# Kernel tuning notes

Hardware: AMD Instinct MI355X
Metric: run time of the kernel (lower is better)

## Reference

```python
import jax, jax.numpy as jnp
import numpy as np

INPUT, OUTPUT, HIDDEN, EMBED = 20000, 2048, 1024, 512
BATCH, NUM_GENES = 512, 20000

def _linear_init(key, fan_in, fan_out):
    kw, kb = jax.random.split(key)
    bound = 1.0 / np.sqrt(fan_in)
    W = jax.random.uniform(kw, (fan_out, fan_in), minval=-bound, maxval=bound, dtype=jnp.float32)
    b = jax.random.uniform(kb, (fan_out,), minval=-bound, maxval=bound, dtype=jnp.float32)
    return W, b

def setup_inputs() -> dict:
    key = jax.random.key(0)
    kx, ke, k1, k2, k3 = jax.random.split(key, 5)
    x = jax.random.normal(kx, (BATCH, INPUT), dtype=jnp.float32)
    embedding_x = jax.random.normal(ke, (NUM_GENES, EMBED), dtype=jnp.float32)
    W_ge, b_ge = _linear_init(k1, INPUT, HIDDEN)   # gene_expander Linear
    W_em, b_em = _linear_init(k2, EMBED, HIDDEN)   # embed_mlp Linear
    W_c, b_c = _linear_init(k3, 2 * HIDDEN, OUTPUT)  # combiner Linear
    return {"x": x, "embedding_x": embedding_x, "W_ge": W_ge, "b_ge": b_ge,
            "W_em": W_em, "b_em": b_em, "W_c": W_c, "b_c": b_c}

def reference(x, embedding_x, W_ge, b_ge, W_em, b_em, W_c, b_c):
    lrelu = lambda v: jax.nn.leaky_relu(v, negative_slope=0.01)
    # gene_expander: [B, input] -> [B, hidden]
    x_expanded = lrelu(x @ W_ge.T + b_ge)
    # embed_mlp (dropout = identity at eval): [G, embed] -> [G, hidden]
    gene_embeddings = lrelu(embedding_x @ W_em.T + b_em)
    # softmax over features, then batched GEMM replaces the per-sample loop
    num_genes = min(x.shape[1], gene_embeddings.shape[0])
    weights = jax.nn.softmax(x, axis=1)
    weighted_embeddings = weights[:, :num_genes] @ gene_embeddings[:num_genes]  # [B, hidden]
    combined = jnp.concatenate([x_expanded, weighted_embeddings], axis=1)  # [B, 2*hidden]
    return lrelu(combined @ W_c.T + b_c)  # [B, output]
```

## Files before the change

### kernel.cpp

```cpp
#include <hip/hip_runtime.h>
#include <hip/hip_bf16.h>
#include <stdint.h>

#define BATCH  512
#define INPUT  20000
#define KPAD   20032
#define NPADE  20224
#define HIDDEN 1024
#define EMBED  512
#define NOUT   2048

typedef __attribute__((ext_vector_type(8))) __bf16 bf16x8;
typedef __attribute__((ext_vector_type(8))) unsigned short u16x8;
typedef __attribute__((ext_vector_type(4))) unsigned short u16x4;
typedef __attribute__((ext_vector_type(4))) float f32x4;

static __device__ __forceinline__ unsigned short f2bf(float f) {
  uint32_t u = __builtin_bit_cast(uint32_t, f);
  u += 0x7fffu + ((u >> 16) & 1u);
  return (unsigned short)(u >> 16);
}

static __device__ __forceinline__ void g2l16(const unsigned short* g, unsigned short* l) {
  __builtin_amdgcn_global_load_lds(
      (const __attribute__((address_space(1))) void*)g,
      (__attribute__((address_space(3))) void*)l, 16, 0, 0);
}

#define MFMA(a, b, c) __builtin_amdgcn_mfma_f32_16x16x32_bf16((a), (b), (c), 0, 0, 0)

template<int EPI>
__global__ __launch_bounds__(512, 2) void gemm8p(
    const unsigned short* __restrict__ A0p, const unsigned short* __restrict__ B0p,
    const unsigned short* __restrict__ A1p, const unsigned short* __restrict__ B1p,
    int lda, int ldb,
    const float* __restrict__ bias,
    void* __restrict__ Cp, int ldc,
    int Nv, int Nw, int K, int kChunk)
{
  __shared__ __align__(16) unsigned short As[2][2][128 * 64];
  __shared__ __align__(16) unsigned short Bs[2][2][128 * 64];
  unsigned short* AsW = &As[0][0][0];
  unsigned short* BsW = &Bs[0][0][0];

  const int zall  = blockIdx.z;
  const int which = (EPI == 1) ? (zall >> 4) : 0;
  const int z     = (EPI == 1) ? (zall & 15) : 0;
  const unsigned short* Ap = which ? A1p : A0p;
  const unsigned short* Bp = which ? B1p : B0p;

  const int m0 = blockIdx.y * 256, n0 = blockIdx.x * 256;
  const int k0   = z * kChunk;
  const int kend = min(K, k0 + kChunk);
  const int nt   = (kend - k0) >> 6;

  const int tid = threadIdx.x;
  const int l = tid & 63, w = tid >> 6;
  const int srow = tid >> 3;
  const int scol = (((tid & 7) ^ (srow & 7)) << 3);

  const unsigned short* ag = Ap + (size_t)(m0 + srow) * lda + k0 + scol;
  const unsigned short* bg = Bp + (size_t)(n0 + srow) * ldb + k0 + scol;

  const int wr = w >> 2, wc = w & 3;
  const int lr = l & 15, lk = (l >> 4) * 8;
  const int xorv = (lr & 7) * 8;
  const int c0 = lk ^ xorv;
  const int c1 = (32 + lk) ^ xorv;

  auto stA = [&](int buf, int h, int dk) {
    const unsigned short* g = ag + (size_t)(h * 128) * lda + dk;
    unsigned short* d = AsW + (buf * 2 + h) * 8192 + (w * 8) * 64;
    g2l16(g, d);
    g2l16(g + (size_t)64 * lda, d + 64 * 64);
  };
  auto stB = [&](int buf, int h, int dk) {
    const unsigned short* g = bg + (size_t)(h * 128) * ldb + dk;
    unsigned short* d = BsW + (buf * 2 + h) * 8192 + (w * 8) * 64;
    g2l16(g, d);
    g2l16(g + (size_t)64 * ldb, d + 64 * 64);
  };
  auto rdA = [&](int buf, int mi, int ks) -> bf16x8 {
    return *reinterpret_cast<const bf16x8*>(
        AsW + (buf * 2 + wr) * 8192 + (mi * 16 + lr) * 64 + (ks ? c1 : c0));
  };
  auto rdB = [&](int buf, int ni, int ks) -> bf16x8 {
    return *reinterpret_cast<const bf16x8*>(
        BsW + (buf * 2 + (wc >> 1)) * 8192 + ((wc & 1) * 64 + ni * 16 + lr) * 64 + (ks ? c1 : c0));
  };

  f32x4 acc[8][4] = {};

  stA(0, 0, 0); stB(0, 0, 0); stA(0, 1, 0); stB(0, 1, 0);
  if (nt > 1) {
    stA(1, 0, 64); stB(1, 0, 64);
    asm volatile("s_waitcnt vmcnt(4)" ::: "memory");
  } else {
    asm volatile("s_waitcnt vmcnt(0)" ::: "memory");
  }
  __builtin_amdgcn_s_barrier();

  for (int t = 0; t < nt; ++t) {
    const int buf = t & 1, nb = buf ^ 1;
    const int dk1 = (t + 1) << 6, dk2 = (t + 2) << 6;
    bf16x8 a0[4][2], a1[4][2], b0[2][2], b1[2][2];

#pragma unroll
    for (int mi = 0; mi < 4; ++mi) { a0[mi][0] = rdA(buf, mi, 0); a0[mi][1] = rdA(buf, mi, 1); }
#pragma unroll
    for (int ni = 0; ni < 2; ++ni) { b0[ni][0] = rdB(buf, ni, 0); b0[ni][1] = rdB(buf, ni, 1); }
    if (t + 1 < nt) stA(nb, 1, dk1);
    __builtin_amdgcn_s_barrier();
    asm volatile("s_waitcnt lgkmcnt(0)" ::: "memory");
    __builtin_amdgcn_sched_barrier(0);
    __builtin_amdgcn_s_setprio(1);
#pragma unroll
    for (int mi = 0; mi < 4; ++mi)
#pragma unroll
      for (int ni = 0; ni < 2; ++ni) {
        acc[mi][ni] = MFMA(a0[mi][0], b0[ni][0], acc[mi][ni]);
        acc[mi][ni] = MFMA(a0[mi][1], b0[ni][1], acc[mi][ni]);
      }
    __builtin_amdgcn_s_setprio(0);
    __builtin_amdgcn_s_barrier();

#pragma unroll
    for (int mi = 0; mi < 4; ++mi) { a1[mi][0] = rdA(buf, mi + 4, 0); a1[mi][1] = rdA(buf, mi + 4, 1); }
    if (t + 1 < nt) stB(nb, 1, dk1);
    __builtin_amdgcn_s_barrier();
    asm volatile("s_waitcnt lgkmcnt(0)" ::: "memory");
    __builtin_amdgcn_sched_barrier(0);
    __builtin_amdgcn_s_setprio(1);
#pragma unroll
    for (int mi = 0; mi < 4; ++mi)
#pragma unroll
      for (int ni = 0; ni < 2; ++ni) {
        acc[mi + 4][ni] = MFMA(a1[mi][0], b0[ni][0], acc[mi + 4][ni]);
        acc[mi + 4][ni] = MFMA(a1[mi][1], b0[ni][1], acc[mi + 4][ni]);
      }
    __builtin_amdgcn_s_setprio(0);
    __builtin_amdgcn_s_barrier();

#pragma unroll
    for (int ni = 0; ni < 2; ++ni) { b1[ni][0] = rdB(buf, ni + 2, 0); b1[ni][1] = rdB(buf, ni + 2, 1); }
    if (t + 2 < nt) stA(buf, 0, dk2);
    __builtin_amdgcn_s_barrier();
    asm volatile("s_waitcnt lgkmcnt(0)" ::: "memory");
    __builtin_amdgcn_sched_barrier(0);
    __builtin_amdgcn_s_setprio(1);
#pragma unroll
    for (int mi = 0; mi < 4; ++mi)
#pragma unroll
      for (int ni = 0; ni < 2; ++ni) {
        acc[mi + 4][ni + 2] = MFMA(a1[mi][0], b1[ni][0], acc[mi + 4][ni + 2]);
        acc[mi + 4][ni + 2] = MFMA(a1[mi][1], b1[ni][1], acc[mi + 4][ni + 2]);
      }
    __builtin_amdgcn_s_setprio(0);
    __builtin_amdgcn_s_barrier();

    if (t + 2 < nt) stB(buf, 0, dk2);
    __builtin_amdgcn_s_barrier();
    __builtin_amdgcn_sched_barrier(0);
    __builtin_amdgcn_s_setprio(1);
#pragma unroll
    for (int mi = 0; mi < 4; ++mi)
#pragma unroll
      for (int ni = 0; ni < 2; ++ni) {
        acc[mi][ni + 2] = MFMA(a0[mi][0], b1[ni][0], acc[mi][ni + 2]);
        acc[mi][ni + 2] = MFMA(a0[mi][1], b1[ni][1], acc[mi][ni + 2]);
      }
    __builtin_amdgcn_s_setprio(0);
    if (t + 2 < nt)      asm volatile("s_waitcnt vmcnt(4)" ::: "memory");
    else if (t + 1 < nt) asm volatile("s_waitcnt vmcnt(0)" ::: "memory");
    __builtin_amdgcn_s_barrier();
  }

  const int rb = (l >> 4) * 4;
#pragma unroll
  for (int mi = 0; mi < 8; ++mi)
#pragma unroll
    for (int ni = 0; ni < 4; ++ni)
#pragma unroll
      for (int j = 0; j < 4; ++j) {
        int m = m0 + wr * 128 + mi * 16 + rb + j;
        int n = n0 + wc * 64 + ni * 16 + lr;
        float v = acc[mi][ni][j];
        if (EPI == 0) {
          if (n < Nw) {
            float t2 = v + bias[m];
            t2 = t2 > 0.f ? t2 : 0.01f * t2;
            reinterpret_cast<unsigned short*>(Cp)[(size_t)m * ldc + n] =
                (n < Nv) ? f2bf(t2) : (unsigned short)0;
          }
        } else {
          reinterpret_cast<float*>(Cp)[(size_t)z * (BATCH * NOUT) + (size_t)m * ldc +
                                       which * 1024 + n] = v;
        }
      }
}

template<int EPI>
__global__ __launch_bounds__(256) void gemm97(
    const unsigned short* __restrict__ A, const unsigned short* __restrict__ B,
    int lda, int ldb,
    const float* __restrict__ bias,
    void* __restrict__ Cp, int ldc, int pstride,
    int M, int N, int Nw, int K, int kChunk)
{
  __shared__ __align__(16) unsigned short As[128 * 64];
  __shared__ __align__(16) unsigned short Bs[128 * 64];

  const int z = blockIdx.z;
  const int m0 = blockIdx.y * 128, n0 = blockIdx.x * 128;
  const int k0   = z * kChunk;
  const int kend = min(K, k0 + kChunk);
  const int tid = threadIdx.x;
  const int l = tid & 63, w = tid >> 6;

  const int srow = w * 32 + (l >> 3);
  const int scol = (l & 7) * 8;
  const unsigned short* ag = A + (size_t)(m0 + srow) * lda + scol;
  const unsigned short* bg = B + (size_t)(n0 + srow) * ldb + scol;

  const int wm = (w >> 1) * 64, wn = (w & 1) * 64;
  const int lr = l & 15, lk = (l >> 4) * 8;

  f32x4 acc[4][4] = {};

  for (int kb = k0; kb < kend; kb += 64) {
#pragma unroll
    for (int j = 0; j < 4; ++j)
      g2l16(ag + (size_t)j * 8 * lda + kb, As + (w * 32 + j * 8) * 64);
#pragma unroll
    for (int j = 0; j < 4; ++j)
      g2l16(bg + (size_t)j * 8 * ldb + kb, Bs + (w * 32 + j * 8) * 64);
    __syncthreads();
#pragma unroll
    for (int ks = 0; ks < 2; ++ks) {
      bf16x8 a[4], b[4];
#pragma unroll
      for (int i = 0; i < 4; ++i)
        a[i] = *reinterpret_cast<const bf16x8*>(&As[(wm + i * 16 + lr) * 64 + ks * 32 + lk]);
#pragma unroll
      for (int i = 0; i < 4; ++i)
        b[i] = *reinterpret_cast<const bf16x8*>(&Bs[(wn + i * 16 + lr) * 64 + ks * 32 + lk]);
#pragma unroll
      for (int mi = 0; mi < 4; ++mi)
#pragma unroll
        for (int ni = 0; ni < 4; ++ni)
          acc[mi][ni] = MFMA(a[mi], b[ni], acc[mi][ni]);
    }
    __syncthreads();
  }

  const int rb = (l >> 4) * 4;
#pragma unroll
  for (int mi = 0; mi < 4; ++mi) {
#pragma unroll
    for (int ni = 0; ni < 4; ++ni) {
#pragma unroll
      for (int j = 0; j < 4; ++j) {
        int m = m0 + wm + mi * 16 + rb + j;
        int n = n0 + wn + ni * 16 + lr;
        float v = acc[mi][ni][j];
        if (EPI == 0) {
          if (n < Nw) {
            float t = v + bias[m];
            t = t > 0.f ? t : 0.01f * t;
            reinterpret_cast<unsigned short*>(Cp)[(size_t)m * ldc + n] =
                (n < N) ? f2bf(t) : (unsigned short)0;
          }
        } else {
          reinterpret_cast<float*>(Cp)[(size_t)z * pstride + (size_t)m * ldc + n] = v;
        }
      }
    }
  }
}

__global__ __launch_bounds__(256) void convert_kernel(
    const float* __restrict__ src, unsigned short* __restrict__ dst,
    int rows, int cols, int rowsPad, int colsPad)
{
  const int cpc = colsPad >> 3;
  const int nchunks = rowsPad * cpc;
  for (int idx = blockIdx.x * 256 + threadIdx.x; idx < nchunks; idx += gridDim.x * 256) {
    int row = idx / cpc;
    int c0  = (idx - row * cpc) << 3;
    u16x8 v = {};
    if (row < rows && c0 < cols) {
      const float* p = src + (size_t)row * cols + c0;
      f32x4 f0 = *reinterpret_cast<const f32x4*>(p);
      f32x4 f1 = *reinterpret_cast<const f32x4*>(p + 4);
      v[0] = f2bf(f0[0]); v[1] = f2bf(f0[1]); v[2] = f2bf(f0[2]); v[3] = f2bf(f0[3]);
      v[4] = f2bf(f1[0]); v[5] = f2bf(f1[1]); v[6] = f2bf(f1[2]); v[7] = f2bf(f1[3]);
    }
    *reinterpret_cast<u16x8*>(dst + (size_t)row * colsPad + c0) = v;
  }
}

__global__ __launch_bounds__(256) void prep_x_kernel(
    const float* __restrict__ x,
    unsigned short* __restrict__ xb,
    unsigned short* __restrict__ wb)
{
  const int r = blockIdx.x;
  const int t = threadIdx.x;
  const float* xr = x + (size_t)r * INPUT;

  float m = -3.4e38f, s = 0.f;
  for (int c = t; c < INPUT / 4; c += 256) {
    float4 v = reinterpret_cast<const float4*>(xr)[c];
    float cm = fmaxf(fmaxf(v.x, v.y), fmaxf(v.z, v.w));
    if (cm > m) { s *= __expf(m - cm); m = cm; }
    s += __expf(v.x - m) + __expf(v.y - m) + __expf(v.z - m) + __expf(v.w - m);
  }
#pragma unroll
  for (int off = 32; off > 0; off >>= 1) {
    float om = __shfl_xor(m, off);
    float os = __shfl_xor(s, off);
    float nm = fmaxf(m, om);
    s = s * __expf(m - nm) + os * __expf(om - nm);
    m = nm;
  }
  __shared__ float sm[4], ss[4];
  if ((t & 63) == 0) { sm[t >> 6] = m; ss[t >> 6] = s; }
  __syncthreads();
  float M4 = fmaxf(fmaxf(sm[0], sm[1]), fmaxf(sm[2], sm[3]));
  float S4 = ss[0] * __expf(sm[0] - M4) + ss[1] * __expf(sm[1] - M4)
           + ss[2] * __expf(sm[2] - M4) + ss[3] * __expf(sm[3] - M4);
  float inv = 1.f / S4;

  unsigned short* xbr = xb + (size_t)r * KPAD;
  unsigned short* wbr = wb + (size_t)r * KPAD;
  for (int c = t; c < KPAD / 4; c += 256) {
    u16x4 xo = {}, wo = {};
    if (c < INPUT / 4) {
      float4 v = reinterpret_cast<const float4*>(xr)[c];
      xo[0] = f2bf(v.x); xo[1] = f2bf(v.y); xo[2] = f2bf(v.z); xo[3] = f2bf(v.w);
      wo[0] = f2bf(__expf(v.x - M4) * inv);
      wo[1] = f2bf(__expf(v.y - M4) * inv);
      wo[2] = f2bf(__expf(v.z - M4) * inv);
      wo[3] = f2bf(__expf(v.w - M4) * inv);
    }
    reinterpret_cast<u16x4*>(xbr)[c] = xo;
    reinterpret_cast<u16x4*>(wbr)[c] = wo;
  }
}

template<int S, int MODE>
__global__ __launch_bounds__(256) void reduce_kernel(
    const float* __restrict__ P, const float* __restrict__ bias, void* __restrict__ outp)
{
  size_t base = ((size_t)blockIdx.x * 256 + threadIdx.x) * 4;
  f32x4 s = {};
#pragma unroll
  for (int zz = 0; zz < S; ++zz)
    s += *reinterpret_cast<const f32x4*>(P + (size_t)zz * BATCH * NOUT + base);
  int n = (int)(base & (NOUT - 1));
  if (MODE == 0) {
    u16x4 o;
    if (n < 1024) {
#pragma unroll
      for (int j = 0; j < 4; ++j) {
        float v = s[j] + bias[n + j];
        v = v > 0.f ? v : 0.01f * v;
        o[j] = f2bf(v);
      }
    } else {
#pragma unroll
      for (int j = 0; j < 4; ++j) o[j] = f2bf(s[j]);
    }
    *reinterpret_cast<u16x4*>(reinterpret_cast<unsigned short*>(outp) + base) = o;
  } else {
    f32x4 o;
#pragma unroll
    for (int j = 0; j < 4; ++j) {
      float v = s[j] + bias[n + j];
      o[j] = v > 0.f ? v : 0.01f * v;
    }
    *reinterpret_cast<f32x4*>(reinterpret_cast<float*>(outp) + base) = o;
  }
}

extern "C" void kernel_launch(void* const* d_in, const int* in_sizes, int n_in,
                              void* d_out, int out_size, void* d_ws, size_t ws_size,
                              hipStream_t stream)
{
  const float* x    = (const float*)d_in[0];
  const float* emb  = (const float*)d_in[1];
  const float* W_ge = (const float*)d_in[2];
  const float* b_ge = (const float*)d_in[3];
  const float* W_em = (const float*)d_in[4];
  const float* b_em = (const float*)d_in[5];
  const float* W_c  = (const float*)d_in[6];
  const float* b_c  = (const float*)d_in[7];
  float* out = (float*)d_out;

  char* ws = (char*)d_ws;
  unsigned short* xb   = (unsigned short*)(ws);
  unsigned short* wb   = (unsigned short*)(ws + 20512768);
  unsigned short* Wgeb = (unsigned short*)(ws + 41025536);
  unsigned short* Et   = (unsigned short*)(ws + 82051072);
  unsigned short* Wcb  = (unsigned short*)(ws + 123076608);
  unsigned short* comb = (unsigned short*)(ws + 131465216);
  float*          P    = (float*)(ws + 133562368);
  unsigned short* embb = (unsigned short*)(ws + 133562368);
  unsigned short* Wemb = (unsigned short*)(ws + 133562368 + 20709376);

  convert_kernel<<<1024, 256, 0, stream>>>(emb,  embb, INPUT, EMBED, NPADE, EMBED);
  convert_kernel<<<256,  256, 0, stream>>>(W_em, Wemb, HIDDEN, EMBED, HIDDEN, EMBED);
  convert_kernel<<<1024, 256, 0, stream>>>(W_ge, Wgeb, HIDDEN, INPUT, HIDDEN, KPAD);
  convert_kernel<<<512,  256, 0, stream>>>(W_c,  Wcb,  NOUT, NOUT, NOUT, NOUT);

  prep_x_kernel<<<BATCH, 256, 0, stream>>>(x, xb, wb);

  gemm8p<0><<<dim3(79, 4, 1), 512, 0, stream>>>(
      Wemb, embb, nullptr, nullptr, EMBED, EMBED, b_em,
      Et, KPAD, INPUT, KPAD, EMBED, EMBED);

  gemm8p<1><<<dim3(4, 2, 32), 512, 0, stream>>>(
      xb, Wgeb, wb, Et, KPAD, KPAD, nullptr,
      P, NOUT, 0, 0, KPAD, 1280);

  reduce_kernel<16, 0><<<(BATCH * NOUT / 4) / 256, 256, 0, stream>>>(P, b_ge, comb);

  gemm97<1><<<dim3(16, 4, 4), 256, 0, stream>>>(
      comb, Wcb, NOUT, NOUT, nullptr,
      P, NOUT, BATCH * NOUT, BATCH, NOUT, NOUT, NOUT, 512);

  reduce_kernel<4, 1><<<(BATCH * NOUT / 4) / 256, 256, 0, stream>>>(P, b_c, out);
}
```

Measured before the change: 244.3 us.

## Replace direct global-to-LDS pipelined GEMM with register-staged double buffering

Rewrites the main 256x256 bf16 GEMM mainloop. The old version used global_load_lds DMA with an interleaved four-phase schedule, many barriers and setprio. The new one loads the next tile into registers, runs all 64 MFMAs per tile in one block, then writes the registers to the other LDS buffer behind a single __syncthreads. This removes the fine-grained barrier choreography and vmcnt tricks. In exchange it costs extra VGPRs and LDS write instructions, and gives up the overlap between the DMA and the MFMA phases.

```diff
diff --git a/kernel.cpp b/kernel.cpp
--- a/kernel.cpp
+++ b/kernel.cpp
@@ -30,7 +30,7 @@
 #define MFMA(a, b, c) __builtin_amdgcn_mfma_f32_16x16x32_bf16((a), (b), (c), 0, 0, 0)
 
 template<int EPI>
-__global__ __launch_bounds__(512, 2) void gemm8p(
+__global__ __launch_bounds__(512, 2) void gemm8r(
     const unsigned short* __restrict__ A0p, const unsigned short* __restrict__ B0p,
     const unsigned short* __restrict__ A1p, const unsigned short* __restrict__ B1p,
     int lda, int ldb,
@@ -57,10 +57,10 @@
   const int tid = threadIdx.x;
   const int l = tid & 63, w = tid >> 6;
   const int srow = tid >> 3;
-  const int scol = (((tid & 7) ^ (srow & 7)) << 3);
-
-  const unsigned short* ag = Ap + (size_t)(m0 + srow) * lda + k0 + scol;
-  const unsigned short* bg = Bp + (size_t)(n0 + srow) * ldb + k0 + scol;
+  const int sc8  = tid & 7;
+  const unsigned short* agl = Ap + (size_t)(m0 + srow) * lda + k0 + sc8 * 8;
+  const unsigned short* bgl = Bp + (size_t)(n0 + srow) * ldb + k0 + sc8 * 8;
+  const int swc = ((sc8 ^ (srow & 7)) << 3);
 
   const int wr = w >> 2, wc = w & 3;
   const int lr = l & 15, lk = (l >> 4) * 8;
@@ -68,17 +68,11 @@
   const int c0 = lk ^ xorv;
   const int c1 = (32 + lk) ^ xorv;
 
-  auto stA = [&](int buf, int h, int dk) {
-    const unsigned short* g = ag + (size_t)(h * 128) * lda + dk;
-    unsigned short* d = AsW + (buf * 2 + h) * 8192 + (w * 8) * 64;
-    g2l16(g, d);
-    g2l16(g + (size_t)64 * lda, d + 64 * 64);
+  auto ldsA = [&](int buf, int r) -> unsigned short* {
+    return AsW + (buf * 2 + (r >> 7)) * 8192 + (r & 127) * 64 + swc;
   };
-  auto stB = [&](int buf, int h, int dk) {
-    const unsigned short* g = bg + (size_t)(h * 128) * ldb + dk;
-    unsigned short* d = BsW + (buf * 2 + h) * 8192 + (w * 8) * 64;
-    g2l16(g, d);
-    g2l16(g + (size_t)64 * ldb, d + 64 * 64);
+  auto ldsB = [&](int buf, int r) -> unsigned short* {
+    return BsW + (buf * 2 + (r >> 7)) * 8192 + (r & 127) * 64 + swc;
   };
   auto rdA = [&](int buf, int mi, int ks) -> bf16x8 {
     return *reinterpret_cast<const bf16x8*>(
@@ -91,98 +85,68 @@
 
   f32x4 acc[8][4] = {};
 
-  stA(0, 0, 0); stB(0, 0, 0); stA(0, 1, 0); stB(0, 1, 0);
-  if (nt > 1) {
-    stA(1, 0, 64); stB(1, 0, 64);
-    asm volatile("s_waitcnt vmcnt(4)" ::: "memory");
-  } else {
-    asm volatile("s_waitcnt vmcnt(0)" ::: "memory");
-  }
-  __builtin_amdgcn_s_barrier();
+  u16x8 ra0, ra1, ra2, ra3, rb0, rb1, rb2, rb3;
+
+#define LOADT(dk)                                                            \
+  do {                                                                       \
+    ra0 = *reinterpret_cast<const u16x8*>(agl + (size_t)0   * lda + (dk));   \
+    ra1 = *reinterpret_cast<const u16x8*>(agl + (size_t)64  * lda + (dk));   \
+    ra2 = *reinterpret_cast<const u16x8*>(agl + (size_t)128 * lda + (dk));   \
+    ra3 = *reinterpret_cast<const u16x8*>(agl + (size_t)192 * lda + (dk));   \
+    rb0 = *reinterpret_cast<const u16x8*>(bgl + (size_t)0   * ldb + (dk));   \
+    rb1 = *reinterpret_cast<const u16x8*>(bgl + (size_t)64  * ldb + (dk));   \
+    rb2 = *reinterpret_cast<const u16x8*>(bgl + (size_t)128 * ldb + (dk));   \
+    rb3 = *reinterpret_cast<const u16x8*>(bgl + (size_t)192 * ldb + (dk));   \
+  } while (0)
+
+#define WRITET(buf)                                                          \
+  do {                                                                       \
+    *reinterpret_cast<u16x8*>(ldsA(buf, srow))       = ra0;                  \
+    *reinterpret_cast<u16x8*>(ldsA(buf, srow + 64))  = ra1;                  \
+    *reinterpret_cast<u16x8*>(ldsA(buf, srow + 128)) = ra2;                  \
+    *reinterpret_cast<u16x8*>(ldsA(buf, srow + 192)) = ra3;                  \
+    *reinterpret_cast<u16x8*>(ldsB(buf, srow))       = rb0;                  \
+    *reinterpret_cast<u16x8*>(ldsB(buf, srow + 64))  = rb1;                  \
+    *reinterpret_cast<u16x8*>(ldsB(buf, srow + 128)) = rb2;                  \
+    *reinterpret_cast<u16x8*>(ldsB(buf, srow + 192)) = rb3;                  \
+  } while (0)
+
+  LOADT(0);
+  WRITET(0);
+  __syncthreads();
 
   for (int t = 0; t < nt; ++t) {
     const int buf = t & 1, nb = buf ^ 1;
-    const int dk1 = (t + 1) << 6, dk2 = (t + 2) << 6;
-    bf16x8 a0[4][2], a1[4][2], b0[2][2], b1[2][2];
-
-#pragma unroll
-    for (int mi = 0; mi < 4; ++mi) { a0[mi][0] = rdA(buf, mi, 0); a0[mi][1] = rdA(buf, mi, 1); }
-#pragma unroll
-    for (int ni = 0; ni < 2; ++ni) { b0[ni][0] = rdB(buf, ni, 0); b0[ni][1] = rdB(buf, ni, 1); }
-    if (t + 1 < nt) stA(nb, 1, dk1);
-    __builtin_amdgcn_s_barrier();
-    asm volatile("s_waitcnt lgkmcnt(0)" ::: "memory");
+    if (t + 1 < nt) LOADT((t + 1) << 6);
     __builtin_amdgcn_sched_barrier(0);
-    __builtin_amdgcn_s_setprio(1);
-#pragma unroll
-    for (int mi = 0; mi < 4; ++mi)
-#pragma unroll
-      for (int ni = 0; ni < 2; ++ni) {
-        acc[mi][ni] = MFMA(a0[mi][0], b0[ni][0], acc[mi][ni]);
-        acc[mi][ni] = MFMA(a0[mi][1], b0[ni][1], acc[mi][ni]);
+
+    bf16x8 a[8][2], b[4][2];
+#pragma unroll
+    for (int mi = 0; mi < 8; ++mi) { a[mi][0] = rdA(buf, mi, 0); a[mi][1] = rdA(buf, mi, 1); }
+#pragma unroll
+    for (int ni = 0; ni < 4; ++ni) { b[ni][0] = rdB(buf, ni, 0); b[ni][1] = rdB(buf, ni, 1); }
+#pragma unroll
+    for (int mi = 0; mi < 8; ++mi)
+#pragma unroll
+      for (int ni = 0; ni < 4; ++ni) {
+        acc[mi][ni] = MFMA(a[mi][0], b[ni][0], acc[mi][ni]);
+        acc[mi][ni] = MFMA(a[mi][1], b[ni][1], acc[mi][ni]);
       }
-    __builtin_amdgcn_s_setprio(0);
-    __builtin_amdgcn_s_barrier();
-
-#pragma unroll
-    for (int mi = 0; mi < 4; ++mi) { a1[mi][0] = rdA(buf, mi + 4, 0); a1[mi][1] = rdA(buf, mi + 4, 1); }
-    if (t + 1 < nt) stB(nb, 1, dk1);
-    __builtin_amdgcn_s_barrier();
-    asm volatile("s_waitcnt lgkmcnt(0)" ::: "memory");
-    __builtin_amdgcn_sched_barrier(0);
-    __builtin_amdgcn_s_setprio(1);
-#pragma unroll
-    for (int mi = 0; mi < 4; ++mi)
-#pragma unroll
-      for (int ni = 0; ni < 2; ++ni) {
-        acc[mi + 4][ni] = MFMA(a1[mi][0], b0[ni][0], acc[mi + 4][ni]);
-        acc[mi + 4][ni] = MFMA(a1[mi][1], b0[ni][1], acc[mi + 4][ni]);
-      }
-    __builtin_amdgcn_s_setprio(0);
-    __builtin_amdgcn_s_barrier();
-
-#pragma unroll
-    for (int ni = 0; ni < 2; ++ni) { b1[ni][0] = rdB(buf, ni + 2, 0); b1[ni][1] = rdB(buf, ni + 2, 1); }
-    if (t + 2 < nt) stA(buf, 0, dk2);
-    __builtin_amdgcn_s_barrier();
-    asm volatile("s_waitcnt lgkmcnt(0)" ::: "memory");
-    __builtin_amdgcn_sched_barrier(0);
-    __builtin_amdgcn_s_setprio(1);
-#pragma unroll
-    for (int mi = 0; mi < 4; ++mi)
-#pragma unroll
-      for (int ni = 0; ni < 2; ++ni) {
-        acc[mi + 4][ni + 2] = MFMA(a1[mi][0], b1[ni][0], acc[mi + 4][ni + 2]);
-        acc[mi + 4][ni + 2] = MFMA(a1[mi][1], b1[ni][1], acc[mi + 4][ni + 2]);
-      }
-    __builtin_amdgcn_s_setprio(0);
-    __builtin_amdgcn_s_barrier();
-
-    if (t + 2 < nt) stB(buf, 0, dk2);
-    __builtin_amdgcn_s_barrier();
-    __builtin_amdgcn_sched_barrier(0);
-    __builtin_amdgcn_s_setprio(1);
-#pragma unroll
-    for (int mi = 0; mi < 4; ++mi)
-#pragma unroll
-      for (int ni = 0; ni < 2; ++ni) {
-        acc[mi][ni + 2] = MFMA(a0[mi][0], b1[ni][0], acc[mi][ni + 2]);
-        acc[mi][ni + 2] = MFMA(a0[mi][1], b1[ni][1], acc[mi][ni + 2]);
-      }
-    __builtin_amdgcn_s_setprio(0);
-    if (t + 2 < nt)      asm volatile("s_waitcnt vmcnt(4)" ::: "memory");
-    else if (t + 1 < nt) asm volatile("s_waitcnt vmcnt(0)" ::: "memory");
-    __builtin_amdgcn_s_barrier();
-  }
-
-  const int rb = (l >> 4) * 4;
+
+    if (t + 1 < nt) WRITET(nb);
+    __syncthreads();
+  }
+#undef LOADT
+#undef WRITET
+
+  const int rb_ = (l >> 4) * 4;
 #pragma unroll
   for (int mi = 0; mi < 8; ++mi)
 #pragma unroll
     for (int ni = 0; ni < 4; ++ni)
 #pragma unroll
       for (int j = 0; j < 4; ++j) {
-        int m = m0 + wr * 128 + mi * 16 + rb + j;
+        int m = m0 + wr * 128 + mi * 16 + rb_ + j;
         int n = n0 + wc * 64 + ni * 16 + lr;
         float v = acc[mi][ni][j];
         if (EPI == 0) {
@@ -415,11 +379,11 @@
 
   prep_x_kernel<<<BATCH, 256, 0, stream>>>(x, xb, wb);
 
-  gemm8p<0><<<dim3(79, 4, 1), 512, 0, stream>>>(
+  gemm8r<0><<<dim3(79, 4, 1), 512, 0, stream>>>(
       Wemb, embb, nullptr, nullptr, EMBED, EMBED, b_em,
       Et, KPAD, INPUT, KPAD, EMBED, EMBED);
 
-  gemm8p<1><<<dim3(4, 2, 32), 512, 0, stream>>>(
+  gemm8r<1><<<dim3(4, 2, 32), 512, 0, stream>>>(
       xb, Wgeb, wb, Et, KPAD, KPAD, nullptr,
       P, NOUT, 0, 0, KPAD, 1280);
 
```

Result: no change. 241.7 us, median of 4 (-1.1%).
